# Kernel tuning notes

Measured on AMD Instinct MI355X. Metric: run time of the kernel, lower is better.

Reference implementation:

```python
import jax, jax.numpy as jnp
import numpy as np

EPS = 0.01          # halting threshold eps
MAX_STEPS = 16      # static cap on the data-dependent while-loop (bias=1.0 halts in ~2 steps)


def setup_inputs() -> dict:
    key = jax.random.key(0)
    ks = jax.random.split(key, 10)
    I, H, O = 4096, 4096, 4096
    sc = 1.0 / np.sqrt(H)
    u = lambda k, shape: jax.random.uniform(k, shape, jnp.float32, -sc, sc)
    return {
        "x": jax.random.normal(ks[0], (I,), jnp.float32),
        "s": jax.random.normal(ks[1], (H,), jnp.float32) * 0.1,
        "W_ih": u(ks[2], (H, 1 + I)),   # nn.RNN weight_ih_l0
        "b_ih": u(ks[3], (H,)),
        "W_hh": u(ks[4], (H, H)),       # nn.RNN weight_hh_l0
        "b_hh": u(ks[5], (H,)),
        "w_halt": u(ks[6], (1, H)),     # fc_halt.weight
        "b_halt": jnp.array([1.0], jnp.float32),  # fc_halt.bias init per module
        "W_out": u(ks[7], (O, H)),      # fc_output.weight
        "b_out": u(ks[8], (O,)),
    }


def reference(x, s, W_ih, b_ih, W_hh, b_hh, w_halt, b_halt, W_out, b_out):
    # x1 = [1, x] for the first step, x0 = [0, x] for subsequent steps
    x0 = jnp.concatenate([jnp.zeros((1,), x.dtype), x])
    x1 = jnp.concatenate([jnp.ones((1,), x.dtype), x])

    def step(h, t):
        xin = jnp.where(t == 0, x1, x0)
        # torch nn.RNN (tanh) cell: h' = tanh(W_ih x + b_ih + W_hh h + b_hh)
        h = jnp.tanh(W_ih @ xin + b_ih + W_hh @ h + b_hh)
        out = W_out @ h + b_out                 # fc_output
        p = jax.nn.sigmoid(w_halt @ h + b_halt)[0]  # fc_halt -> sigmoid
        return h, (h, out, p)

    _, (hs, outs, ps) = jax.lax.scan(step, s, jnp.arange(MAX_STEPS))
    # accumulated halting probability; loop stops at first step with cum >= 1-eps.
    cum = jnp.cumsum(ps)
    crossed = cum >= 1.0 - EPS
    # Binarize: only the first crossing step gets 1 (cum is strictly increasing,
    # and the original while-loop exits there), so mv with the binarized vector
    # selects outputs/states at step N, and ponder = sum(1 - bin) = N.
    N = jnp.where(jnp.any(crossed), jnp.argmax(crossed), MAX_STEPS - 1)
    output = outs[N]
    s_new = hs[N]
    ponder = N.astype(x.dtype)
    return output, s_new, ponder
```

## Files before the change

kernel.cpp:

```cpp
#include <hip/hip_runtime.h>
#include <hip/hip_cooperative_groups.h>

namespace cg = cooperative_groups;

static constexpr int   H         = 4096;
static constexpr int   MAX_STEPS = 16;
static constexpr float EPS       = 0.01f;

__device__ __forceinline__ float wave_reduce(float v) {
    #pragma unroll
    for (int off = 32; off > 0; off >>= 1) v += __shfl_down(v, off);
    return v;
}
__device__ __forceinline__ float sigmoidf(float z) { return 1.f / (1.f + __expf(-z)); }

static constexpr int TPB_C = 1024;
static constexpr int NB_C  = 256;
static constexpr int CWS_H    = 0;
static constexpr int CWS_PART = 2 * H;

__global__ void __launch_bounds__(TPB_C, 4)
k_fused(const float* __restrict__ x,     const float* __restrict__ s,
        const float* __restrict__ Wih,   const float* __restrict__ bih,
        const float* __restrict__ Whh,   const float* __restrict__ bhh,
        const float* __restrict__ whalt, const float* __restrict__ bhalt,
        const float* __restrict__ Wout,  const float* __restrict__ bout,
        float* __restrict__ ws,          float* __restrict__ out)
{
    cg::grid_group grid = cg::this_grid();
    __shared__ float sh[H];
    __shared__ float hred[16];
    const int tid = threadIdx.x, lane = tid & 63, wave = tid >> 6;
    const int row = blockIdx.x * 16 + wave;
    float* wsH  = ws + CWS_H;
    float* part = ws + CWS_PART;
    const float bh = bhalt[0];

    for (int i = tid; i < H / 4; i += TPB_C)
        ((float4*)sh)[i] = ((const float4*)x)[i];
    __syncthreads();

    const long long off0 = (long long)row * (H + 1) + 1;
    const int a = (int)((4 - (off0 & 3)) & 3);
    float acc = 0.f;
    if (lane < a) acc += Wih[off0 + lane] * sh[lane];
    const int nvec = (H - a) >> 2;
    const float4* wv = (const float4*)(Wih + off0 + a);
    for (int i = lane; i < nvec; i += 64) {
        float4 w  = wv[i];
        const int e = a + i * 4;
        acc = fmaf(w.x, sh[e],     acc);
        acc = fmaf(w.y, sh[e + 1], acc);
        acc = fmaf(w.z, sh[e + 2], acc);
        acc = fmaf(w.w, sh[e + 3], acc);
    }
    const int tail  = (H - a) & 3;
    const int tbase = a + nvec * 4;
    if (lane < tail) acc += Wih[off0 + tbase + lane] * sh[tbase + lane];
    acc = wave_reduce(acc);
    float v0 = 0.f, wih0 = 0.f;
    if (lane == 0) {
        v0   = acc + bih[row] + bhh[row];
        wih0 = Wih[(long long)row * (H + 1)];
    }
    __syncthreads();

    int   N   = MAX_STEPS - 1;
    float cum = 0.f;
    for (int t = 0; t < MAX_STEPS; ++t) {
        const float* hin = (t == 0) ? s : (wsH + (size_t)(t & 1) * H);
        for (int i = tid; i < H / 4; i += TPB_C)
            ((float4*)sh)[i] = ((const float4*)hin)[i];
        __syncthreads();

        const float4* Wr = (const float4*)(Whh + (size_t)row * H);
        float4 w[16];
        #pragma unroll
        for (int it = 0; it < 16; ++it) w[it] = Wr[it * 64 + lane];
        float a2 = 0.f;
        #pragma unroll
        for (int it = 0; it < 16; ++it) {
            float4 hv = ((const float4*)sh)[it * 64 + lane];
            a2 = fmaf(w[it].x, hv.x, a2);
            a2 = fmaf(w[it].y, hv.y, a2);
            a2 = fmaf(w[it].z, hv.z, a2);
            a2 = fmaf(w[it].w, hv.w, a2);
        }
        a2 = wave_reduce(a2);
        if (lane == 0) {
            float pre  = a2 + v0 + (t == 0 ? wih0 : 0.f);
            float hval = tanhf(pre);
            wsH[(size_t)((t + 1) & 1) * H + row] = hval;
            hred[wave] = whalt[row] * hval;
        }
        __syncthreads();
        if (tid == 0) {
            float v = 0.f;
            #pragma unroll
            for (int j2 = 0; j2 < 16; ++j2) v += hred[j2];
            part[t * NB_C + blockIdx.x] = v;
        }
        __threadfence();
        grid.sync();

        float sl = (tid < NB_C) ? part[t * NB_C + tid] : 0.f;
        sl = wave_reduce(sl);
        if (lane == 0) hred[wave] = sl;
        __syncthreads();
        float sj = 0.f;
        #pragma unroll
        for (int j2 = 0; j2 < 16; ++j2) sj += hred[j2];
        cum += sigmoidf(sj + bh);
        __syncthreads();
        if (cum >= 1.f - EPS) { N = t; break; }
    }

    const float* hN = wsH + (size_t)((N + 1) & 1) * H;
    for (int i = tid; i < H / 4; i += TPB_C)
        ((float4*)sh)[i] = ((const float4*)hN)[i];
    __syncthreads();

    const float4* Wr = (const float4*)(Wout + (size_t)row * H);
    float4 w[16];
    #pragma unroll
    for (int it = 0; it < 16; ++it) w[it] = Wr[it * 64 + lane];
    float a3 = 0.f;
    #pragma unroll
    for (int it = 0; it < 16; ++it) {
        float4 hv = ((const float4*)sh)[it * 64 + lane];
        a3 = fmaf(w[it].x, hv.x, a3);
        a3 = fmaf(w[it].y, hv.y, a3);
        a3 = fmaf(w[it].z, hv.z, a3);
        a3 = fmaf(w[it].w, hv.w, a3);
    }
    a3 = wave_reduce(a3);
    if (lane == 0) {
        out[row]     = a3 + bout[row];
        out[H + row] = sh[row];
        if (row == 0) out[2 * H] = (float)N;
    }
}

static constexpr int TPB         = 256;
static constexpr int NB          = H / 4;
static constexpr int SLOTS       = 64;
static constexpr int SLOT_STRIDE = 32;

static constexpr int FWS_V0   = 0;
static constexpr int FWS_WIH0 = H;
static constexpr int FWS_TOT  = 2 * H;
static constexpr int FWS_PART = 2 * H + 32;
static constexpr int FWS_H    = FWS_PART + MAX_STEPS * SLOTS * SLOT_STRIDE;

__global__ void __launch_bounds__(TPB)
k_init(const float* __restrict__ x, const float* __restrict__ s,
       const float* __restrict__ Wih, const float* __restrict__ bih,
       const float* __restrict__ bhh, float* __restrict__ ws)
{
    __shared__ float xs[H];
    const int tid = threadIdx.x, lane = tid & 63, wave = tid >> 6;
    const int row = blockIdx.x * 4 + wave;

    for (int i = tid; i < H / 4; i += TPB)
        ((float4*)xs)[i] = ((const float4*)x)[i];
    __syncthreads();

    const long long off0 = (long long)row * (H + 1) + 1;
    const int a = (int)((4 - (off0 & 3)) & 3);
    float acc = 0.f;
    if (lane < a) acc += Wih[off0 + lane] * xs[lane];
    const int nvec = (H - a) >> 2;
    const float4* wv = (const float4*)(Wih + off0 + a);
    for (int i = lane; i < nvec; i += 64) {
        float4 w  = wv[i];
        const int e = a + i * 4;
        acc = fmaf(w.x, xs[e],     acc);
        acc = fmaf(w.y, xs[e + 1], acc);
        acc = fmaf(w.z, xs[e + 2], acc);
        acc = fmaf(w.w, xs[e + 3], acc);
    }
    const int tail  = (H - a) & 3;
    const int tbase = a + nvec * 4;
    if (lane < tail) acc += Wih[off0 + tbase + lane] * xs[tbase + lane];
    acc = wave_reduce(acc);
    if (lane == 0) {
        ws[FWS_V0 + row]   = acc + bih[row] + bhh[row];
        ws[FWS_WIH0 + row] = Wih[(long long)row * (H + 1)];
    }

    const int gid = blockIdx.x * TPB + tid;
    if (gid < H) ws[FWS_H + gid] = s[gid];
    if (gid < 32 + MAX_STEPS * SLOTS * SLOT_STRIDE)
        ws[FWS_TOT + gid] = 0.f;
}

__global__ void __launch_bounds__(TPB, 4)
k_step(int t, const float* __restrict__ Whh, const float* __restrict__ whalt,
       const float* __restrict__ bhalt, float* __restrict__ ws)
{
    const float bh = bhalt[0];

    float cum = 0.f;
    for (int j = 0; j < t - 1; ++j) {
        cum += sigmoidf(ws[FWS_TOT + j] + bh);
        if (cum >= 1.f - EPS) return;
    }
    if (t >= 1) {
        float sj = 0.f;
        const float* p = ws + FWS_PART + (size_t)(t - 1) * (SLOTS * SLOT_STRIDE);
        #pragma unroll
        for (int g = 0; g < SLOTS; ++g) sj += p[g * SLOT_STRIDE];
        if (threadIdx.x == 0) ws[FWS_TOT + (t - 1)] = sj;
        cum += sigmoidf(sj + bh);
        if (cum >= 1.f - EPS) return;
    }

    __shared__ float hs[H];
    __shared__ float hred[4];
    const int tid = threadIdx.x, lane = tid & 63, wave = tid >> 6;
    const float* hin  = ws + FWS_H + (size_t)(t & 1) * H;
    float*       hout = ws + FWS_H + (size_t)((t + 1) & 1) * H;
    for (int i = tid; i < H / 4; i += TPB)
        ((float4*)hs)[i] = ((const float4*)hin)[i];
    __syncthreads();

    const int row = blockIdx.x * 4 + wave;
    const float4* Wr = (const float4*)(Whh + (size_t)row * H);
    float4 w[16];
    #pragma unroll
    for (int it = 0; it < 16; ++it) w[it] = Wr[it * 64 + lane];
    float acc = 0.f;
    #pragma unroll
    for (int it = 0; it < 16; ++it) {
        float4 hv = ((const float4*)hs)[it * 64 + lane];
        acc = fmaf(w[it].x, hv.x, acc);
        acc = fmaf(w[it].y, hv.y, acc);
        acc = fmaf(w[it].z, hv.z, acc);
        acc = fmaf(w[it].w, hv.w, acc);
    }
    acc = wave_reduce(acc);
    if (lane == 0) {
        float pre  = acc + ws[FWS_V0 + row] + (t == 0 ? ws[FWS_WIH0 + row] : 0.f);
        float hval = tanhf(pre);
        hout[row]  = hval;
        hred[wave] = whalt[row] * hval;
    }
    __syncthreads();
    if (tid == 0) {
        float v = hred[0] + hred[1] + hred[2] + hred[3];
        atomicAdd(&ws[FWS_PART + (size_t)t * (SLOTS * SLOT_STRIDE)
                      + (blockIdx.x & (SLOTS - 1)) * SLOT_STRIDE], v);
    }
}

__global__ void __launch_bounds__(TPB, 4)
k_final(const float* __restrict__ Wout, const float* __restrict__ bout,
        const float* __restrict__ bhalt, float* __restrict__ ws,
        float* __restrict__ out)
{
    const float bh = bhalt[0];
    float cum = 0.f;
    int N = MAX_STEPS - 1;
    for (int j = 0; j < MAX_STEPS; ++j) {
        float sj;
        if (j < MAX_STEPS - 1) sj = ws[FWS_TOT + j];
        else {
            sj = 0.f;
            const float* p = ws + FWS_PART + (size_t)(MAX_STEPS - 1) * (SLOTS * SLOT_STRIDE);
            #pragma unroll
            for (int g = 0; g < SLOTS; ++g) sj += p[g * SLOT_STRIDE];
        }
        cum += sigmoidf(sj + bh);
        if (cum >= 1.f - EPS) { N = j; break; }
    }

    __shared__ float hs[H];
    const float* hN = ws + FWS_H + (size_t)((N + 1) & 1) * H;
    const int tid = threadIdx.x, lane = tid & 63, wave = tid >> 6;
    for (int i = tid; i < H / 4; i += TPB)
        ((float4*)hs)[i] = ((const float4*)hN)[i];
    __syncthreads();

    const int row = blockIdx.x * 4 + wave;
    const float4* Wr = (const float4*)(Wout + (size_t)row * H);
    float4 w[16];
    #pragma unroll
    for (int it = 0; it < 16; ++it) w[it] = Wr[it * 64 + lane];
    float acc = 0.f;
    #pragma unroll
    for (int it = 0; it < 16; ++it) {
        float4 hv = ((const float4*)hs)[it * 64 + lane];
        acc = fmaf(w[it].x, hv.x, acc);
        acc = fmaf(w[it].y, hv.y, acc);
        acc = fmaf(w[it].z, hv.z, acc);
        acc = fmaf(w[it].w, hv.w, acc);
    }
    acc = wave_reduce(acc);
    if (lane == 0) {
        out[row]     = acc + bout[row];
        out[H + row] = hs[row];
        if (row == 0) out[2 * H] = (float)N;
    }
}

extern "C" void kernel_launch(void* const* d_in, const int* in_sizes, int n_in,
                              void* d_out, int out_size, void* d_ws, size_t ws_size,
                              hipStream_t stream) {
    const float* x     = (const float*)d_in[0];
    const float* s     = (const float*)d_in[1];
    const float* Wih   = (const float*)d_in[2];
    const float* bih   = (const float*)d_in[3];
    const float* Whh   = (const float*)d_in[4];
    const float* bhh   = (const float*)d_in[5];
    const float* whalt = (const float*)d_in[6];
    const float* bhalt = (const float*)d_in[7];
    const float* Wout  = (const float*)d_in[8];
    const float* bout  = (const float*)d_in[9];
    float* out = (float*)d_out;
    float* ws  = (float*)d_ws;

    static int use_coop = -1;
    if (use_coop < 0) {
        int dev = 0;  (void)hipGetDevice(&dev);
        int coop = 0; (void)hipDeviceGetAttribute(&coop, hipDeviceAttributeCooperativeLaunch, dev);
        int ncu = 0;  (void)hipDeviceGetAttribute(&ncu, hipDeviceAttributeMultiprocessorCount, dev);
        int maxb = 0;
        (void)hipOccupancyMaxActiveBlocksPerMultiprocessor(&maxb, k_fused, TPB_C, 0);
        use_coop = (coop != 0 && (long long)maxb * (long long)ncu >= NB_C) ? 1 : 0;
    }

    if (use_coop == 1) {
        void* args[] = { &x, &s, &Wih, &bih, &Whh, &bhh, &whalt, &bhalt,
                         &Wout, &bout, &ws, &out };
        hipError_t e = hipLaunchCooperativeKernel((const void*)k_fused, dim3(NB_C),
                                                  dim3(TPB_C), args, 0, stream);
        if (e == hipSuccess) return;
        use_coop = 0;
    }

    k_init<<<NB, TPB, 0, stream>>>(x, s, Wih, bih, bhh, ws);
    for (int t = 0; t < MAX_STEPS; ++t)
        k_step<<<NB, TPB, 0, stream>>>(t, Whh, whalt, bhalt, ws);
    k_final<<<NB, TPB, 0, stream>>>(Wout, bout, bhalt, ws, out);
}
```

Measured before the change: 258.4 us.

## Split first two RNN steps into regular kernels before cooperative tail

Replaces the single cooperative kernel with two ordinary 1024-block kernels for steps 0 and 1, with the kernel boundary acting as the grid barrier. The Wih and first Whh matvecs are fused into one kernel. A cooperative tail kernel then continues steps 2 and later only if not yet halted, and computes the output projection. This is meant to cut grid.sync overhead and spread the early work over more blocks, at the cost of two extra launches. If the cooperative launch fails, the fallback path reruns everything after the first two kernels have already written the workspace.

After: 259.9 us. No clear change (+0.6%).

```diff
diff --git a/kernel.cpp b/kernel.cpp
--- a/kernel.cpp
+++ b/kernel.cpp
@@ -7,6 +7,18 @@
 static constexpr int   MAX_STEPS = 16;
 static constexpr float EPS       = 0.01f;
 
+static constexpr int TPB   = 256;
+static constexpr int NB    = H / 4;
+static constexpr int TPB_C = 1024;
+static constexpr int NB_C  = 256;
+
+static constexpr int WS_V0   = 0;
+static constexpr int WS_HB   = H;
+static constexpr int WS_P0   = 3 * H;
+static constexpr int WS_P1   = 3 * H + NB;
+static constexpr int WS_PC   = 3 * H + 2 * NB;
+static constexpr int WS_CTRL = WS_PC + MAX_STEPS * NB_C;
+
 __device__ __forceinline__ float wave_reduce(float v) {
     #pragma unroll
     for (int off = 32; off > 0; off >>= 1) v += __shfl_down(v, off);
@@ -14,108 +26,206 @@
 }
 __device__ __forceinline__ float sigmoidf(float z) { return 1.f / (1.f + __expf(-z)); }
 
-static constexpr int TPB_C = 1024;
-static constexpr int NB_C  = 256;
-static constexpr int CWS_H    = 0;
-static constexpr int CWS_PART = 2 * H;
-
-__global__ void __launch_bounds__(TPB_C, 4)
-k_fused(const float* __restrict__ x,     const float* __restrict__ s,
-        const float* __restrict__ Wih,   const float* __restrict__ bih,
-        const float* __restrict__ Whh,   const float* __restrict__ bhh,
-        const float* __restrict__ whalt, const float* __restrict__ bhalt,
-        const float* __restrict__ Wout,  const float* __restrict__ bout,
-        float* __restrict__ ws,          float* __restrict__ out)
-{
-    cg::grid_group grid = cg::this_grid();
-    __shared__ float sh[H];
-    __shared__ float hred[16];
-    const int tid = threadIdx.x, lane = tid & 63, wave = tid >> 6;
-    const int row = blockIdx.x * 16 + wave;
-    float* wsH  = ws + CWS_H;
-    float* part = ws + CWS_PART;
-    const float bh = bhalt[0];
-
-    for (int i = tid; i < H / 4; i += TPB_C)
-        ((float4*)sh)[i] = ((const float4*)x)[i];
+__global__ void __launch_bounds__(TPB, 4)
+k_init0(const float* __restrict__ x,   const float* __restrict__ s,
+        const float* __restrict__ Wih, const float* __restrict__ bih,
+        const float* __restrict__ Whh, const float* __restrict__ bhh,
+        const float* __restrict__ whalt, float* __restrict__ ws)
+{
+    __shared__ float xs[H];
+    __shared__ float ss[H];
+    __shared__ float hred[4];
+    const int tid = threadIdx.x, lane = tid & 63, wave = tid >> 6;
+    const int row = blockIdx.x * 4 + wave;
+
+    for (int i = tid; i < H / 4; i += TPB) {
+        ((float4*)xs)[i] = ((const float4*)x)[i];
+        ((float4*)ss)[i] = ((const float4*)s)[i];
+    }
     __syncthreads();
 
     const long long off0 = (long long)row * (H + 1) + 1;
     const int a = (int)((4 - (off0 & 3)) & 3);
-    float acc = 0.f;
-    if (lane < a) acc += Wih[off0 + lane] * sh[lane];
+    float acc_ih = 0.f;
+    if (lane < a) acc_ih += Wih[off0 + lane] * xs[lane];
     const int nvec = (H - a) >> 2;
     const float4* wv = (const float4*)(Wih + off0 + a);
     for (int i = lane; i < nvec; i += 64) {
         float4 w  = wv[i];
         const int e = a + i * 4;
-        acc = fmaf(w.x, sh[e],     acc);
-        acc = fmaf(w.y, sh[e + 1], acc);
-        acc = fmaf(w.z, sh[e + 2], acc);
-        acc = fmaf(w.w, sh[e + 3], acc);
+        acc_ih = fmaf(w.x, xs[e],     acc_ih);
+        acc_ih = fmaf(w.y, xs[e + 1], acc_ih);
+        acc_ih = fmaf(w.z, xs[e + 2], acc_ih);
+        acc_ih = fmaf(w.w, xs[e + 3], acc_ih);
     }
     const int tail  = (H - a) & 3;
     const int tbase = a + nvec * 4;
-    if (lane < tail) acc += Wih[off0 + tbase + lane] * sh[tbase + lane];
+    if (lane < tail) acc_ih += Wih[off0 + tbase + lane] * xs[tbase + lane];
+    acc_ih = wave_reduce(acc_ih);
+
+    const float4* Wr = (const float4*)(Whh + (size_t)row * H);
+    float4 w[16];
+    #pragma unroll
+    for (int it = 0; it < 16; ++it) w[it] = Wr[it * 64 + lane];
+    float acc_hh = 0.f;
+    #pragma unroll
+    for (int it = 0; it < 16; ++it) {
+        float4 hv = ((const float4*)ss)[it * 64 + lane];
+        acc_hh = fmaf(w[it].x, hv.x, acc_hh);
+        acc_hh = fmaf(w[it].y, hv.y, acc_hh);
+        acc_hh = fmaf(w[it].z, hv.z, acc_hh);
+        acc_hh = fmaf(w[it].w, hv.w, acc_hh);
+    }
+    acc_hh = wave_reduce(acc_hh);
+
+    if (lane == 0) {
+        const float v0 = acc_ih + bih[row] + bhh[row];
+        ws[WS_V0 + row] = v0;
+        const float wih0 = Wih[(long long)row * (H + 1)];
+        const float h1 = tanhf(v0 + wih0 + acc_hh);
+        ws[WS_HB + 1 * H + row] = h1;
+        hred[wave] = whalt[row] * h1;
+    }
+    __syncthreads();
+    if (tid == 0)
+        ws[WS_P0 + blockIdx.x] = hred[0] + hred[1] + hred[2] + hred[3];
+}
+
+__global__ void __launch_bounds__(TPB, 4)
+k_step1(const float* __restrict__ Whh, const float* __restrict__ whalt,
+        const float* __restrict__ bhalt, float* __restrict__ ws)
+{
+    __shared__ float hs[H];
+    __shared__ float hred[4];
+    const int tid = threadIdx.x, lane = tid & 63, wave = tid >> 6;
+    const float bh = bhalt[0];
+
+    float p = 0.f;
+    #pragma unroll
+    for (int k = 0; k < NB / TPB; ++k) p += ws[WS_P0 + tid + k * TPB];
+    p = wave_reduce(p);
+    if (lane == 0) hred[wave] = p;
+    __syncthreads();
+    const float total0 = hred[0] + hred[1] + hred[2] + hred[3];
+    const float cum0 = sigmoidf(total0 + bh);
+    const bool halted0 = (cum0 >= 1.f - EPS);
+    if (blockIdx.x == 0 && tid == 0) {
+        ws[WS_CTRL]     = halted0 ? 0.f : -1.f;
+        ws[WS_CTRL + 1] = cum0;
+    }
+    if (halted0) return;
+    __syncthreads();
+
+    const float* hin = ws + WS_HB + 1 * H;
+    for (int i = tid; i < H / 4; i += TPB)
+        ((float4*)hs)[i] = ((const float4*)hin)[i];
+    __syncthreads();
+
+    const int row = blockIdx.x * 4 + wave;
+    const float4* Wr = (const float4*)(Whh + (size_t)row * H);
+    float4 w[16];
+    #pragma unroll
+    for (int it = 0; it < 16; ++it) w[it] = Wr[it * 64 + lane];
+    float acc = 0.f;
+    #pragma unroll
+    for (int it = 0; it < 16; ++it) {
+        float4 hv = ((const float4*)hs)[it * 64 + lane];
+        acc = fmaf(w[it].x, hv.x, acc);
+        acc = fmaf(w[it].y, hv.y, acc);
+        acc = fmaf(w[it].z, hv.z, acc);
+        acc = fmaf(w[it].w, hv.w, acc);
+    }
     acc = wave_reduce(acc);
-    float v0 = 0.f, wih0 = 0.f;
-    if (lane == 0) {
-        v0   = acc + bih[row] + bhh[row];
-        wih0 = Wih[(long long)row * (H + 1)];
-    }
-    __syncthreads();
-
-    int   N   = MAX_STEPS - 1;
-    float cum = 0.f;
-    for (int t = 0; t < MAX_STEPS; ++t) {
-        const float* hin = (t == 0) ? s : (wsH + (size_t)(t & 1) * H);
-        for (int i = tid; i < H / 4; i += TPB_C)
-            ((float4*)sh)[i] = ((const float4*)hin)[i];
+    if (lane == 0) {
+        const float h2 = tanhf(acc + ws[WS_V0 + row]);
+        ws[WS_HB + 0 * H + row] = h2;
+        hred[wave] = whalt[row] * h2;
+    }
+    __syncthreads();
+    if (tid == 0)
+        ws[WS_P1 + blockIdx.x] = hred[0] + hred[1] + hred[2] + hred[3];
+}
+
+__global__ void __launch_bounds__(TPB_C, 4)
+k_tail(const float* __restrict__ Whh,   const float* __restrict__ whalt,
+       const float* __restrict__ bhalt, const float* __restrict__ Wout,
+       const float* __restrict__ bout,  float* __restrict__ ws,
+       float* __restrict__ out)
+{
+    cg::grid_group grid = cg::this_grid();
+    __shared__ float sh[H];
+    __shared__ float hred[16];
+    const int tid = threadIdx.x, lane = tid & 63, wave = tid >> 6;
+    const int row = blockIdx.x * 16 + wave;
+    const float bh = bhalt[0];
+
+    const float ctrl0 = ws[WS_CTRL];
+    int N;
+    if (ctrl0 >= 0.f) {
+        N = (int)ctrl0;
+    } else {
+        float p = ws[WS_P1 + tid];
+        p = wave_reduce(p);
+        if (lane == 0) hred[wave] = p;
         __syncthreads();
-
-        const float4* Wr = (const float4*)(Whh + (size_t)row * H);
-        float4 w[16];
+        float total1 = 0.f;
         #pragma unroll
-        for (int it = 0; it < 16; ++it) w[it] = Wr[it * 64 + lane];
-        float a2 = 0.f;
-        #pragma unroll
-        for (int it = 0; it < 16; ++it) {
-            float4 hv = ((const float4*)sh)[it * 64 + lane];
-            a2 = fmaf(w[it].x, hv.x, a2);
-            a2 = fmaf(w[it].y, hv.y, a2);
-            a2 = fmaf(w[it].z, hv.z, a2);
-            a2 = fmaf(w[it].w, hv.w, a2);
+        for (int j = 0; j < 16; ++j) total1 += hred[j];
+        float cum = ws[WS_CTRL + 1] + sigmoidf(total1 + bh);
+        __syncthreads();
+        if (cum >= 1.f - EPS) {
+            N = 1;
+        } else {
+            N = MAX_STEPS - 1;
+            for (int t = 2; t < MAX_STEPS; ++t) {
+                const float* hin = ws + WS_HB + (size_t)(t & 1) * H;
+                for (int i = tid; i < H / 4; i += TPB_C)
+                    ((float4*)sh)[i] = ((const float4*)hin)[i];
+                __syncthreads();
+
+                const float4* Wr = (const float4*)(Whh + (size_t)row * H);
+                float4 w[16];
+                #pragma unroll
+                for (int it = 0; it < 16; ++it) w[it] = Wr[it * 64 + lane];
+                float a2 = 0.f;
+                #pragma unroll
+                for (int it = 0; it < 16; ++it) {
+                    float4 hv = ((const float4*)sh)[it * 64 + lane];
+                    a2 = fmaf(w[it].x, hv.x, a2);
+                    a2 = fmaf(w[it].y, hv.y, a2);
+                    a2 = fmaf(w[it].z, hv.z, a2);
+                    a2 = fmaf(w[it].w, hv.w, a2);
+                }
+                a2 = wave_reduce(a2);
+                if (lane == 0) {
+                    const float hval = tanhf(a2 + ws[WS_V0 + row]);
+                    ws[WS_HB + (size_t)((t + 1) & 1) * H + row] = hval;
+                    hred[wave] = whalt[row] * hval;
+                }
+                __syncthreads();
+                if (tid == 0) {
+                    float v = 0.f;
+                    #pragma unroll
+                    for (int j = 0; j < 16; ++j) v += hred[j];
+                    ws[WS_PC + t * NB_C + blockIdx.x] = v;
+                }
+                grid.sync();
+
+                float q = (tid < NB_C) ? ws[WS_PC + t * NB_C + tid] : 0.f;
+                q = wave_reduce(q);
+                if (lane == 0) hred[wave] = q;
+                __syncthreads();
+                float tot = 0.f;
+                #pragma unroll
+                for (int j = 0; j < 16; ++j) tot += hred[j];
+                cum += sigmoidf(tot + bh);
+                __syncthreads();
+                if (cum >= 1.f - EPS) { N = t; break; }
+            }
         }
-        a2 = wave_reduce(a2);
-        if (lane == 0) {
-            float pre  = a2 + v0 + (t == 0 ? wih0 : 0.f);
-            float hval = tanhf(pre);
-            wsH[(size_t)((t + 1) & 1) * H + row] = hval;
-            hred[wave] = whalt[row] * hval;
-        }
-        __syncthreads();
-        if (tid == 0) {
-            float v = 0.f;
-            #pragma unroll
-            for (int j2 = 0; j2 < 16; ++j2) v += hred[j2];
-            part[t * NB_C + blockIdx.x] = v;
-        }
-        __threadfence();
-        grid.sync();
-
-        float sl = (tid < NB_C) ? part[t * NB_C + tid] : 0.f;
-        sl = wave_reduce(sl);
-        if (lane == 0) hred[wave] = sl;
-        __syncthreads();
-        float sj = 0.f;
-        #pragma unroll
-        for (int j2 = 0; j2 < 16; ++j2) sj += hred[j2];
-        cum += sigmoidf(sj + bh);
-        __syncthreads();
-        if (cum >= 1.f - EPS) { N = t; break; }
-    }
-
-    const float* hN = wsH + (size_t)((N + 1) & 1) * H;
+    }
+
+    const float* hN = ws + WS_HB + (size_t)((N + 1) & 1) * H;
     for (int i = tid; i < H / 4; i += TPB_C)
         ((float4*)sh)[i] = ((const float4*)hN)[i];
     __syncthreads();
@@ -141,11 +251,8 @@
     }
 }
 
-static constexpr int TPB         = 256;
-static constexpr int NB          = H / 4;
 static constexpr int SLOTS       = 64;
 static constexpr int SLOT_STRIDE = 32;
-
 static constexpr int FWS_V0   = 0;
 static constexpr int FWS_WIH0 = H;
 static constexpr int FWS_TOT  = 2 * H;
@@ -187,11 +294,9 @@
         ws[FWS_V0 + row]   = acc + bih[row] + bhh[row];
         ws[FWS_WIH0 + row] = Wih[(long long)row * (H + 1)];
     }
-
     const int gid = blockIdx.x * TPB + tid;
     if (gid < H) ws[FWS_H + gid] = s[gid];
-    if (gid < 32 + MAX_STEPS * SLOTS * SLOT_STRIDE)
-        ws[FWS_TOT + gid] = 0.f;
+    if (gid < 32 + MAX_STEPS * SLOTS * SLOT_STRIDE) ws[FWS_TOT + gid] = 0.f;
 }
 
 __global__ void __launch_bounds__(TPB, 4)
@@ -199,7 +304,6 @@
        const float* __restrict__ bhalt, float* __restrict__ ws)
 {
     const float bh = bhalt[0];
-
     float cum = 0.f;
     for (int j = 0; j < t - 1; ++j) {
         cum += sigmoidf(ws[FWS_TOT + j] + bh);
@@ -325,14 +429,15 @@
         int coop = 0; (void)hipDeviceGetAttribute(&coop, hipDeviceAttributeCooperativeLaunch, dev);
         int ncu = 0;  (void)hipDeviceGetAttribute(&ncu, hipDeviceAttributeMultiprocessorCount, dev);
         int maxb = 0;
-        (void)hipOccupancyMaxActiveBlocksPerMultiprocessor(&maxb, k_fused, TPB_C, 0);
+        (void)hipOccupancyMaxActiveBlocksPerMultiprocessor(&maxb, k_tail, TPB_C, 0);
         use_coop = (coop != 0 && (long long)maxb * (long long)ncu >= NB_C) ? 1 : 0;
     }
 
     if (use_coop == 1) {
-        void* args[] = { &x, &s, &Wih, &bih, &Whh, &bhh, &whalt, &bhalt,
-                         &Wout, &bout, &ws, &out };
-        hipError_t e = hipLaunchCooperativeKernel((const void*)k_fused, dim3(NB_C),
+        k_init0<<<NB, TPB, 0, stream>>>(x, s, Wih, bih, Whh, bhh, whalt, ws);
+        k_step1<<<NB, TPB, 0, stream>>>(Whh, whalt, bhalt, ws);
+        void* args[] = { &Whh, &whalt, &bhalt, &Wout, &bout, &ws, &out };
+        hipError_t e = hipLaunchCooperativeKernel((const void*)k_tail, dim3(NB_C),
                                                   dim3(TPB_C), args, 0, stream);
         if (e == hipSuccess) return;
         use_coop = 0;
```
